# Kernel tuning notes

Hardware: AMD Instinct MI355X
Metric: run time of the kernel (lower is better)

Reference implementation:

```python
import jax, jax.numpy as jnp
import numpy as np

EMBED = 768
CROSS = 512
HEADS = 12
HDIM = EMBED // HEADS
FFN = 4 * EMBED
B, S, L = 8, 1024, 256
EPS = 1e-5


def setup_inputs() -> dict:
    key = jax.random.key(0)
    ks = iter(jax.random.split(key, 40))
    r = lambda shape, s=0.02: jax.random.normal(next(ks), shape, dtype=jnp.float32) * s
    inp = {
        'hidden_state': jax.random.normal(next(ks), (B, S, EMBED), dtype=jnp.float32),
        'context': jax.random.normal(next(ks), (B, L, CROSS), dtype=jnp.float32),
        # cross_norm
        'cn_g': jnp.ones((EMBED,), jnp.float32), 'cn_b': jnp.zeros((EMBED,), jnp.float32),
        # cross attention projections
        'wq_c': r((EMBED, EMBED)), 'bq_c': jnp.zeros((EMBED,), jnp.float32),
        'wk_c': r((CROSS, EMBED)), 'bk_c': jnp.zeros((EMBED,), jnp.float32),
        'wv_c': r((CROSS, EMBED)), 'bv_c': jnp.zeros((EMBED,), jnp.float32),
        'wo_c': r((EMBED, EMBED)), 'bo_c': jnp.zeros((EMBED,), jnp.float32),
        'bias_c': r((HEADS, S, L)),  # relative position bias (cross)
        # self_norm
        'sn_g': jnp.ones((EMBED,), jnp.float32), 'sn_b': jnp.zeros((EMBED,), jnp.float32),
        # self attention projections
        'wq_s': r((EMBED, EMBED)), 'bq_s': jnp.zeros((EMBED,), jnp.float32),
        'wk_s': r((EMBED, EMBED)), 'bk_s': jnp.zeros((EMBED,), jnp.float32),
        'wv_s': r((EMBED, EMBED)), 'bv_s': jnp.zeros((EMBED,), jnp.float32),
        'wo_s': r((EMBED, EMBED)), 'bo_s': jnp.zeros((EMBED,), jnp.float32),
        'bias_s': r((HEADS, S, S)),  # relative position bias (self)
        # ffn_norm
        'fn_g': jnp.ones((EMBED,), jnp.float32), 'fn_b': jnp.zeros((EMBED,), jnp.float32),
        # FFN
        'w1': r((EMBED, FFN)), 'b1': jnp.zeros((FFN,), jnp.float32),
        'w2': r((FFN, EMBED)), 'b2': jnp.zeros((EMBED,), jnp.float32),
    }
    return inp


def _ln(x, g, b):
    mu = jnp.mean(x, axis=-1, keepdims=True)
    var = jnp.mean(jnp.square(x - mu), axis=-1, keepdims=True)
    return (x - mu) * jax.lax.rsqrt(var + EPS) * g + b


def _heads(x):  # [B,T,E] -> [B,H,T,D]
    b, t, _ = x.shape
    return x.reshape(b, t, HEADS, HDIM).transpose(0, 2, 1, 3)


def _attn(xq, xkv, wq, bq, wk, bk, wv, bv, wo, bo, bias):
    q = _heads(xq @ wq + bq)
    k = _heads(xkv @ wk + bk)
    v = _heads(xkv @ wv + bv)
    scale = 1.0 / jnp.sqrt(jnp.asarray(HDIM, q.dtype))
    scores = jnp.einsum('bhqd,bhkd->bhqk', q, k) * scale + bias[None]
    p = jax.nn.softmax(scores, axis=-1)
    o = jnp.einsum('bhqk,bhkd->bhqd', p, v)
    b_, _, t, _ = o.shape
    o = o.transpose(0, 2, 1, 3).reshape(b_, t, EMBED)
    return o @ wo + bo


def reference(hidden_state, context, cn_g, cn_b, wq_c, bq_c, wk_c, bk_c, wv_c, bv_c,
              wo_c, bo_c, bias_c, sn_g, sn_b, wq_s, bq_s, wk_s, bk_s, wv_s, bv_s,
              wo_s, bo_s, bias_s, fn_g, fn_b, w1, b1, w2, b2):
    h = _attn(_ln(hidden_state, cn_g, cn_b), context,
              wq_c, bq_c, wk_c, bk_c, wv_c, bv_c, wo_c, bo_c, bias_c) + hidden_state
    h = _attn(_ln(h, sn_g, sn_b), _ln(h, sn_g, sn_b),
              wq_s, bq_s, wk_s, bk_s, wv_s, bv_s, wo_s, bo_s, bias_s) + h
    y = _ln(h, fn_g, fn_b)
    y = jax.nn.gelu(y @ w1 + b1) @ w2 + b2  # NOTE: original has no residual after FFN
    return y
```

## Files before the change

### kernel.cpp

```cpp
#include <hip/hip_runtime.h>
#include <hip/hip_bf16.h>
#include <math.h>

#define EMBED 768
#define CROSS 512
#define HEADS 12
#define HDIM  64
#define FFN_DIM 3072
#define BATCH 8
#define SEQ   1024
#define CTX   256
#define LN_EPS 1e-5f

using f32x4 = __attribute__((ext_vector_type(4))) float;
using s16x8 = __attribute__((ext_vector_type(8))) short;

__device__ __forceinline__ unsigned short f2bf(float f) {
    union { float f; unsigned u; } x{f};
    const unsigned r = x.u + 0x7fffu + ((x.u >> 16) & 1u);
    return (unsigned short)(r >> 16);
}

__device__ __forceinline__ void gl16(const void* g, void* l) {
    __builtin_amdgcn_global_load_lds(
        (const __attribute__((address_space(1))) void*)g,
        (__attribute__((address_space(3))) void*)l, 16, 0, 0);
}

__device__ __forceinline__ float gelu_f(float x) {
    const float c = 0.7978845608028654f;
    return 0.5f * x * (1.0f + tanhf(c * (x + 0.044715f * x * x * x)));
}

__global__ __launch_bounds__(256) void transpose_cast_kernel(
    const float* __restrict__ W, unsigned short* __restrict__ WT, int K, int N)
{
    __shared__ float T[32][33];
    const int k0 = blockIdx.y * 32, n0 = blockIdx.x * 32;
    const int t = threadIdx.x;
    const int r = t >> 3, c4 = (t & 7) * 4;
    const float4 v = *(const float4*)(W + (size_t)(k0 + r) * N + n0 + c4);
    T[r][c4 + 0] = v.x; T[r][c4 + 1] = v.y; T[r][c4 + 2] = v.z; T[r][c4 + 3] = v.w;
    __syncthreads();
    ushort4 o;
    o.x = f2bf(T[c4 + 0][r]); o.y = f2bf(T[c4 + 1][r]);
    o.z = f2bf(T[c4 + 2][r]); o.w = f2bf(T[c4 + 3][r]);
    *(ushort4*)(WT + (size_t)(n0 + r) * K + k0 + c4) = o;
}

__global__ __launch_bounds__(256) void cast_bf16_kernel(
    const float* __restrict__ x, unsigned short* __restrict__ y, int n)
{
    const int i = (blockIdx.x * 256 + threadIdx.x) * 4;
    if (i < n) {
        const float4 v = *(const float4*)(x + i);
        ushort4 o{f2bf(v.x), f2bf(v.y), f2bf(v.z), f2bf(v.w)};
        *(ushort4*)(y + i) = o;
    }
}

__global__ __launch_bounds__(256) void ln_kernel(
    const float* __restrict__ x, const float* __restrict__ g,
    const float* __restrict__ beta, unsigned short* __restrict__ y)
{
    __shared__ float red[256];
    const size_t row = blockIdx.x;
    const float* xr = x + row * EMBED;
    const int t = threadIdx.x;

    float v0 = xr[t], v1 = xr[t + 256], v2 = xr[t + 512];

    red[t] = v0 + v1 + v2;
    __syncthreads();
    for (int off = 128; off > 0; off >>= 1) {
        if (t < off) red[t] += red[t + off];
        __syncthreads();
    }
    const float mu = red[0] * (1.0f / (float)EMBED);
    __syncthreads();

    const float d0 = v0 - mu, d1 = v1 - mu, d2 = v2 - mu;
    red[t] = d0 * d0 + d1 * d1 + d2 * d2;
    __syncthreads();
    for (int off = 128; off > 0; off >>= 1) {
        if (t < off) red[t] += red[t + off];
        __syncthreads();
    }
    const float var = red[0] * (1.0f / (float)EMBED);
    const float rstd = rsqrtf(var + LN_EPS);

    unsigned short* yr = y + row * EMBED;
    yr[t]       = f2bf(d0 * rstd * g[t]       + beta[t]);
    yr[t + 256] = f2bf(d1 * rstd * g[t + 256] + beta[t + 256]);
    yr[t + 512] = f2bf(d2 * rstd * g[t + 512] + beta[t + 512]);
}

template <int MODE, int DO_GELU>
__global__ __launch_bounds__(256) void gemm_mfma_kernel(
    const unsigned short* __restrict__ A,
    const unsigned short* __restrict__ WT,
    const float* __restrict__ bias,
    const float* __restrict__ resid,
    void* __restrict__ Cv, int M, int N, int K, int sklog)
{
    __shared__ unsigned short As[128][32];
    __shared__ unsigned short Bs[128][32];

    const int t = threadIdx.x;
    const int l = t & 63;
    const int w = t >> 6;
    const int m0 = blockIdx.y * 128;
    const int n0 = blockIdx.x * 128;
    const int wm = (w >> 1) * 64;
    const int wn = (w & 1) * 64;

    const int sr = t >> 2;
    const int sc = t & 3;

    f32x4 acc[4][4] = {};

    const unsigned short* Ap0 = A  + (size_t)(m0 + sr) * K + sc * 8;
    const unsigned short* Ap1 = Ap0 + (size_t)64 * K;
    const unsigned short* Bp0 = WT + (size_t)(n0 + sr) * K + sc * 8;
    const unsigned short* Bp1 = Bp0 + (size_t)64 * K;

    const int fr = l & 15;
    const int kb = (l >> 4) * 8;

    for (int k0 = 0; k0 < K; k0 += 32) {
        gl16(Ap0 + k0, &As[sr][sc * 8]);
        gl16(Ap1 + k0, &As[sr + 64][sc * 8]);
        gl16(Bp0 + k0, &Bs[sr][sc * 8]);
        gl16(Bp1 + k0, &Bs[sr + 64][sc * 8]);
        __syncthreads();

        s16x8 af[4], bf[4];
#pragma unroll
        for (int i = 0; i < 4; ++i) af[i] = *(const s16x8*)&As[wm + i * 16 + fr][kb];
#pragma unroll
        for (int j = 0; j < 4; ++j) bf[j] = *(const s16x8*)&Bs[wn + j * 16 + fr][kb];
#pragma unroll
        for (int i = 0; i < 4; ++i)
#pragma unroll
            for (int j = 0; j < 4; ++j)
                acc[i][j] = __builtin_amdgcn_mfma_f32_16x16x32_bf16(
                    af[i], bf[j], acc[i][j], 0, 0, 0);
        __syncthreads();
    }

    const int rg = (l >> 4) * 4;
#pragma unroll
    for (int j = 0; j < 4; ++j) {
        const int col = n0 + wn + j * 16 + fr;
        const float bia = bias[col];
#pragma unroll
        for (int i = 0; i < 4; ++i) {
#pragma unroll
            for (int r = 0; r < 4; ++r) {
                const int row = m0 + wm + i * 16 + rg + r;
                float v = acc[i][j][r] + bia;
                if (resid) v += resid[(size_t)row * N + col];
                if (DO_GELU) v = gelu_f(v);
                if (MODE == 0) {
                    ((float*)Cv)[(size_t)row * N + col] = v;
                } else if (MODE == 1) {
                    ((unsigned short*)Cv)[(size_t)row * N + col] = f2bf(v);
                } else {
                    const int bb = row >> sklog;
                    const int kk = row - (bb << sklog);
                    const int hh = col >> 6;
                    const int dd = col & 63;
                    ((unsigned short*)Cv)[
                        (((size_t)(bb * HEADS + hh) * 64 + dd) << sklog) + kk] = f2bf(v);
                }
            }
        }
    }
}

template <int SK>
__global__ __launch_bounds__(256) void flash_mfma_kernel(
    const unsigned short* __restrict__ Q, const unsigned short* __restrict__ K,
    const unsigned short* __restrict__ VT, const float* __restrict__ bias,
    unsigned short* __restrict__ O, float scale)
{
    __shared__ unsigned short Qs[64][72];
    __shared__ unsigned short Ks[64][72];
    __shared__ unsigned short Vts[64][72];
    __shared__ unsigned short Ps[64][72];

    const int g = blockIdx.x;
    const int L = (g & 7) * 192 + (g >> 3);
    const int b  = L & 7;
    const int qt = (L >> 3) & 15;
    const int h  = L >> 7;
    const int q0 = qt * 64;

    const int t  = threadIdx.x;
    const int l  = t & 63;
    const int w  = t >> 6;
    const int fr = l & 15;
    const int hi = l >> 4;

    const int str = t >> 3;
    const int stc = (t & 7) * 8;

#pragma unroll
    for (int ps = 0; ps < 2; ++ps) {
        const int r = str + ps * 32;
        *(uint4*)&Qs[r][stc] =
            *(const uint4*)(Q + ((size_t)(b * SEQ) + q0 + r) * EMBED + h * HDIM + stc);
    }

    float m_[4], l_[4];
    f32x4 o_[4];
#pragma unroll
    for (int r = 0; r < 4; ++r) { m_[r] = -1e30f; l_[r] = 0.0f; }
#pragma unroll
    for (int n = 0; n < 4; ++n) o_[n] = f32x4{0.f, 0.f, 0.f, 0.f};

    const float* bbase = bias + ((size_t)h * SEQ + q0 + w * 16) * SK;

    for (int k0 = 0; k0 < SK; k0 += 64) {
#pragma unroll
        for (int ps = 0; ps < 2; ++ps) {
            const int r = str + ps * 32;
            *(uint4*)&Ks[r][stc] =
                *(const uint4*)(K + ((size_t)(b * SK) + k0 + r) * EMBED + h * HDIM + stc);
            *(uint4*)&Vts[r][stc] =
                *(const uint4*)(VT + ((size_t)(b * HEADS + h) * 64 + r) * SK + k0 + stc);
        }
        __syncthreads();

        f32x4 s[4] = {};
#pragma unroll
        for (int ks = 0; ks < 2; ++ks) {
            const s16x8 aq = *(const s16x8*)&Qs[w * 16 + fr][ks * 32 + hi * 8];
#pragma unroll
            for (int j = 0; j < 4; ++j) {
                const s16x8 bk = *(const s16x8*)&Ks[j * 16 + fr][ks * 32 + hi * 8];
                s[j] = __builtin_amdgcn_mfma_f32_16x16x32_bf16(aq, bk, s[j], 0, 0, 0);
            }
        }

        float corr[4];
#pragma unroll
        for (int r = 0; r < 4; ++r) {
            const float* br = bbase + (size_t)(hi * 4 + r) * SK + k0 + fr;
            float v0 = s[0][r] * scale + br[0];
            float v1 = s[1][r] * scale + br[16];
            float v2 = s[2][r] * scale + br[32];
            float v3 = s[3][r] * scale + br[48];
            float mx = fmaxf(fmaxf(v0, v1), fmaxf(v2, v3));
            mx = fmaxf(mx, __shfl_xor(mx, 1));
            mx = fmaxf(mx, __shfl_xor(mx, 2));
            mx = fmaxf(mx, __shfl_xor(mx, 4));
            mx = fmaxf(mx, __shfl_xor(mx, 8));
            const float mnew = fmaxf(m_[r], mx);
            const float c = __expf(m_[r] - mnew);
            m_[r] = mnew;
            const float p0 = __expf(v0 - mnew);
            const float p1 = __expf(v1 - mnew);
            const float p2 = __expf(v2 - mnew);
            const float p3 = __expf(v3 - mnew);
            float psum = p0 + p1 + p2 + p3;
            psum += __shfl_xor(psum, 1);
            psum += __shfl_xor(psum, 2);
            psum += __shfl_xor(psum, 4);
            psum += __shfl_xor(psum, 8);
            l_[r] = l_[r] * c + psum;
            corr[r] = c;
            const int prow = w * 16 + hi * 4 + r;
            Ps[prow][fr]      = f2bf(p0);
            Ps[prow][fr + 16] = f2bf(p1);
            Ps[prow][fr + 32] = f2bf(p2);
            Ps[prow][fr + 48] = f2bf(p3);
        }
#pragma unroll
        for (int n = 0; n < 4; ++n)
#pragma unroll
            for (int r = 0; r < 4; ++r) o_[n][r] *= corr[r];

#pragma unroll
        for (int ks = 0; ks < 2; ++ks) {
            const s16x8 ap = *(const s16x8*)&Ps[w * 16 + fr][ks * 32 + hi * 8];
#pragma unroll
            for (int n = 0; n < 4; ++n) {
                const s16x8 bv = *(const s16x8*)&Vts[n * 16 + fr][ks * 32 + hi * 8];
                o_[n] = __builtin_amdgcn_mfma_f32_16x16x32_bf16(ap, bv, o_[n], 0, 0, 0);
            }
        }
        __syncthreads();
    }

    float inv[4];
#pragma unroll
    for (int r = 0; r < 4; ++r) inv[r] = 1.0f / l_[r];
#pragma unroll
    for (int n = 0; n < 4; ++n)
#pragma unroll
        for (int r = 0; r < 4; ++r)
            O[((size_t)(b * SEQ) + q0 + w * 16 + hi * 4 + r) * EMBED +
              h * HDIM + n * 16 + fr] = f2bf(o_[n][r] * inv[r]);
}

extern "C" void kernel_launch(void* const* d_in, const int* in_sizes, int n_in,
                              void* d_out, int out_size, void* d_ws, size_t ws_size,
                              hipStream_t stream)
{
    const float* hidden  = (const float*)d_in[0];
    const float* context = (const float*)d_in[1];
    const float* cn_g = (const float*)d_in[2];
    const float* cn_b = (const float*)d_in[3];
    const float* wq_c = (const float*)d_in[4];
    const float* bq_c = (const float*)d_in[5];
    const float* wk_c = (const float*)d_in[6];
    const float* bk_c = (const float*)d_in[7];
    const float* wv_c = (const float*)d_in[8];
    const float* bv_c = (const float*)d_in[9];
    const float* wo_c = (const float*)d_in[10];
    const float* bo_c = (const float*)d_in[11];
    const float* bias_c = (const float*)d_in[12];
    const float* sn_g = (const float*)d_in[13];
    const float* sn_b = (const float*)d_in[14];
    const float* wq_s = (const float*)d_in[15];
    const float* bq_s = (const float*)d_in[16];
    const float* wk_s = (const float*)d_in[17];
    const float* bk_s = (const float*)d_in[18];
    const float* wv_s = (const float*)d_in[19];
    const float* bv_s = (const float*)d_in[20];
    const float* wo_s = (const float*)d_in[21];
    const float* bo_s = (const float*)d_in[22];
    const float* bias_s = (const float*)d_in[23];
    const float* fn_g = (const float*)d_in[24];
    const float* fn_b = (const float*)d_in[25];
    const float* w1 = (const float*)d_in[26];
    const float* b1 = (const float*)d_in[27];
    const float* w2 = (const float*)d_in[28];
    const float* b2 = (const float*)d_in[29];

    const size_t NTOK = (size_t)BATCH * SEQ;
    const size_t NCTX = (size_t)BATCH * CTX;
    const size_t TE = NTOK * EMBED;

    char* p = (char*)d_ws;
    float* hbuf = (float*)p;                   p += TE * 4;
    unsigned short* xbuf = (unsigned short*)p; p += TE * 2;
    unsigned short* qbuf = (unsigned short*)p; p += TE * 2;
    unsigned short* kbuf = (unsigned short*)p; p += TE * 2;
    unsigned short* vbuf = (unsigned short*)p; p += TE * 2;
    unsigned short* obuf = (unsigned short*)p; p += TE * 2;
    unsigned short* ctxb = (unsigned short*)p; p += NCTX * CROSS * 2;
    unsigned short* wt_qc = (unsigned short*)p; p += (size_t)EMBED * EMBED * 2;
    unsigned short* wt_kc = (unsigned short*)p; p += (size_t)CROSS * EMBED * 2;
    unsigned short* wt_vc = (unsigned short*)p; p += (size_t)CROSS * EMBED * 2;
    unsigned short* wt_oc = (unsigned short*)p; p += (size_t)EMBED * EMBED * 2;
    unsigned short* wt_qs = (unsigned short*)p; p += (size_t)EMBED * EMBED * 2;
    unsigned short* wt_ks = (unsigned short*)p; p += (size_t)EMBED * EMBED * 2;
    unsigned short* wt_vs = (unsigned short*)p; p += (size_t)EMBED * EMBED * 2;
    unsigned short* wt_os = (unsigned short*)p; p += (size_t)EMBED * EMBED * 2;
    unsigned short* wt_w1 = (unsigned short*)p; p += (size_t)EMBED * FFN_DIM * 2;
    unsigned short* wt_w2 = (unsigned short*)p; p += (size_t)FFN_DIM * EMBED * 2;
    unsigned short* fbuf = qbuf;
    float* out = (float*)d_out;

    const dim3 blk(256);
    const float scale = 0.125f;
    const dim3 agrid(BATCH * (SEQ / 64) * HEADS);

    transpose_cast_kernel<<<dim3(EMBED/32, EMBED/32), blk, 0, stream>>>(wq_c, wt_qc, EMBED, EMBED);
    transpose_cast_kernel<<<dim3(EMBED/32, CROSS/32), blk, 0, stream>>>(wk_c, wt_kc, CROSS, EMBED);
    transpose_cast_kernel<<<dim3(EMBED/32, CROSS/32), blk, 0, stream>>>(wv_c, wt_vc, CROSS, EMBED);
    transpose_cast_kernel<<<dim3(EMBED/32, EMBED/32), blk, 0, stream>>>(wo_c, wt_oc, EMBED, EMBED);
    transpose_cast_kernel<<<dim3(EMBED/32, EMBED/32), blk, 0, stream>>>(wq_s, wt_qs, EMBED, EMBED);
    transpose_cast_kernel<<<dim3(EMBED/32, EMBED/32), blk, 0, stream>>>(wk_s, wt_ks, EMBED, EMBED);
    transpose_cast_kernel<<<dim3(EMBED/32, EMBED/32), blk, 0, stream>>>(wv_s, wt_vs, EMBED, EMBED);
    transpose_cast_kernel<<<dim3(EMBED/32, EMBED/32), blk, 0, stream>>>(wo_s, wt_os, EMBED, EMBED);
    transpose_cast_kernel<<<dim3(FFN_DIM/32, EMBED/32), blk, 0, stream>>>(w1, wt_w1, EMBED, FFN_DIM);
    transpose_cast_kernel<<<dim3(EMBED/32, FFN_DIM/32), blk, 0, stream>>>(w2, wt_w2, FFN_DIM, EMBED);
    cast_bf16_kernel<<<(int)(NCTX * CROSS / 1024), blk, 0, stream>>>(
        context, ctxb, (int)(NCTX * CROSS));

    ln_kernel<<<(int)NTOK, blk, 0, stream>>>(hidden, cn_g, cn_b, xbuf);
    gemm_mfma_kernel<1,0><<<dim3(EMBED/128, NTOK/128), blk, 0, stream>>>(
        xbuf, wt_qc, bq_c, nullptr, qbuf, NTOK, EMBED, EMBED, 0);
    gemm_mfma_kernel<1,0><<<dim3(EMBED/128, NCTX/128), blk, 0, stream>>>(
        ctxb, wt_kc, bk_c, nullptr, kbuf, NCTX, EMBED, CROSS, 0);
    gemm_mfma_kernel<2,0><<<dim3(EMBED/128, NCTX/128), blk, 0, stream>>>(
        ctxb, wt_vc, bv_c, nullptr, vbuf, NCTX, EMBED, CROSS, 8);
    flash_mfma_kernel<CTX><<<agrid, blk, 0, stream>>>(
        qbuf, kbuf, vbuf, bias_c, obuf, scale);
    gemm_mfma_kernel<0,0><<<dim3(EMBED/128, NTOK/128), blk, 0, stream>>>(
        obuf, wt_oc, bo_c, hidden, hbuf, NTOK, EMBED, EMBED, 0);

    ln_kernel<<<(int)NTOK, blk, 0, stream>>>(hbuf, sn_g, sn_b, xbuf);
    gemm_mfma_kernel<1,0><<<dim3(EMBED/128, NTOK/128), blk, 0, stream>>>(
        xbuf, wt_qs, bq_s, nullptr, qbuf, NTOK, EMBED, EMBED, 0);
    gemm_mfma_kernel<1,0><<<dim3(EMBED/128, NTOK/128), blk, 0, stream>>>(
        xbuf, wt_ks, bk_s, nullptr, kbuf, NTOK, EMBED, EMBED, 0);
    gemm_mfma_kernel<2,0><<<dim3(EMBED/128, NTOK/128), blk, 0, stream>>>(
        xbuf, wt_vs, bv_s, nullptr, vbuf, NTOK, EMBED, EMBED, 10);
    flash_mfma_kernel<SEQ><<<agrid, blk, 0, stream>>>(
        qbuf, kbuf, vbuf, bias_s, obuf, scale);
    gemm_mfma_kernel<0,0><<<dim3(EMBED/128, NTOK/128), blk, 0, stream>>>(
        obuf, wt_os, bo_s, hbuf, hbuf, NTOK, EMBED, EMBED, 0);

    ln_kernel<<<(int)NTOK, blk, 0, stream>>>(hbuf, fn_g, fn_b, xbuf);
    gemm_mfma_kernel<1,1><<<dim3(FFN_DIM/128, NTOK/128), blk, 0, stream>>>(
        xbuf, wt_w1, b1, nullptr, fbuf, NTOK, FFN_DIM, EMBED, 0);
    gemm_mfma_kernel<0,0><<<dim3(EMBED/128, NTOK/128), blk, 0, stream>>>(
        fbuf, wt_w2, b2, nullptr, out, NTOK, EMBED, FFN_DIM, 0);
}
```

Before: 828.2 us.

## Fuse QKV projections into one GEMM and prefetch K/V tiles in flash attention

Concatenates the transposed K/V (cross) and Q/K/V (self) weights so that each projection set runs as a single wider GEMM launch, with per-block routing of bias and output (V written transposed). The flash attention kernel now loads the next K/V tile into registers while computing on the current one, and loads the bias values for a tile into registers up front. This removes launch overhead and underfilled grids from the small projection GEMMs and hides global-load latency in attention, at the cost of more registers and an extra barrier per iteration.

```diff
diff --git a/kernel.cpp b/kernel.cpp
--- a/kernel.cpp
+++ b/kernel.cpp
@@ -101,7 +101,7 @@
     const unsigned short* __restrict__ WT,
     const float* __restrict__ bias,
     const float* __restrict__ resid,
-    void* __restrict__ Cv, int M, int N, int K, int sklog)
+    void* __restrict__ Cv, int M, int N, int K)
 {
     __shared__ unsigned short As[128][32];
     __shared__ unsigned short Bs[128][32];
@@ -163,15 +163,91 @@
                 if (DO_GELU) v = gelu_f(v);
                 if (MODE == 0) {
                     ((float*)Cv)[(size_t)row * N + col] = v;
-                } else if (MODE == 1) {
+                } else {
                     ((unsigned short*)Cv)[(size_t)row * N + col] = f2bf(v);
-                } else {
+                }
+            }
+        }
+    }
+}
+
+__global__ __launch_bounds__(256) void gemm_qkv_kernel(
+    const unsigned short* __restrict__ A,
+    const unsigned short* __restrict__ WT,
+    const float* __restrict__ b0, const float* __restrict__ b1,
+    const float* __restrict__ b2,
+    unsigned short* __restrict__ out0, unsigned short* __restrict__ out1,
+    unsigned short* __restrict__ vt,
+    int M, int K, int sklog, int vpart)
+{
+    __shared__ unsigned short As[128][32];
+    __shared__ unsigned short Bs[128][32];
+
+    const int t = threadIdx.x;
+    const int l = t & 63;
+    const int w = t >> 6;
+    const int m0 = blockIdx.y * 128;
+    const int n0 = blockIdx.x * 128;
+    const int part = n0 / 768;
+    const int nl0 = n0 - part * 768;
+    const float* bias = (part == 0) ? b0 : ((part == 1) ? b1 : b2);
+    const int wm = (w >> 1) * 64;
+    const int wn = (w & 1) * 64;
+
+    const int sr = t >> 2;
+    const int sc = t & 3;
+
+    f32x4 acc[4][4] = {};
+
+    const unsigned short* Ap0 = A  + (size_t)(m0 + sr) * K + sc * 8;
+    const unsigned short* Ap1 = Ap0 + (size_t)64 * K;
+    const unsigned short* Bp0 = WT + (size_t)(n0 + sr) * K + sc * 8;
+    const unsigned short* Bp1 = Bp0 + (size_t)64 * K;
+
+    const int fr = l & 15;
+    const int kb = (l >> 4) * 8;
+
+    for (int k0 = 0; k0 < K; k0 += 32) {
+        gl16(Ap0 + k0, &As[sr][sc * 8]);
+        gl16(Ap1 + k0, &As[sr + 64][sc * 8]);
+        gl16(Bp0 + k0, &Bs[sr][sc * 8]);
+        gl16(Bp1 + k0, &Bs[sr + 64][sc * 8]);
+        __syncthreads();
+
+        s16x8 af[4], bf[4];
+#pragma unroll
+        for (int i = 0; i < 4; ++i) af[i] = *(const s16x8*)&As[wm + i * 16 + fr][kb];
+#pragma unroll
+        for (int j = 0; j < 4; ++j) bf[j] = *(const s16x8*)&Bs[wn + j * 16 + fr][kb];
+#pragma unroll
+        for (int i = 0; i < 4; ++i)
+#pragma unroll
+            for (int j = 0; j < 4; ++j)
+                acc[i][j] = __builtin_amdgcn_mfma_f32_16x16x32_bf16(
+                    af[i], bf[j], acc[i][j], 0, 0, 0);
+        __syncthreads();
+    }
+
+    const int rg = (l >> 4) * 4;
+    unsigned short* outp = (part == 0) ? out0 : out1;
+#pragma unroll
+    for (int j = 0; j < 4; ++j) {
+        const int nl = nl0 + wn + j * 16 + fr;
+        const float bia = bias[nl];
+#pragma unroll
+        for (int i = 0; i < 4; ++i) {
+#pragma unroll
+            for (int r = 0; r < 4; ++r) {
+                const int row = m0 + wm + i * 16 + rg + r;
+                const float v = acc[i][j][r] + bia;
+                if (part == vpart) {
                     const int bb = row >> sklog;
                     const int kk = row - (bb << sklog);
-                    const int hh = col >> 6;
-                    const int dd = col & 63;
-                    ((unsigned short*)Cv)[
-                        (((size_t)(bb * HEADS + hh) * 64 + dd) << sklog) + kk] = f2bf(v);
+                    const int hh = nl >> 6;
+                    const int dd = nl & 63;
+                    vt[(((size_t)(bb * HEADS + hh) * 64 + dd) << sklog) + kk] = f2bf(v);
+                } else {
+                    outp[(size_t)row * 768 + nl] = f2bf(v);
                 }
             }
         }
@@ -205,6 +281,8 @@
     const int str = t >> 3;
     const int stc = (t & 7) * 8;
 
+    const unsigned short* Kbase = K + (size_t)(b * SK) * EMBED + h * HDIM + stc;
+
 #pragma unroll
     for (int ps = 0; ps < 2; ++ps) {
         const int r = str + ps * 32;
@@ -212,6 +290,20 @@
             *(const uint4*)(Q + ((size_t)(b * SEQ) + q0 + r) * EMBED + h * HDIM + stc);
     }
 
+    uint4 kreg[2], vreg[2];
+#pragma unroll
+    for (int ps = 0; ps < 2; ++ps) {
+        const int r = str + ps * 32;
+        kreg[ps] = *(const uint4*)(Kbase + (size_t)r * EMBED);
+        vreg[ps] = *(const uint4*)(VT + ((size_t)(b * HEADS + h) * 64 + r) * SK + stc);
+    }
+#pragma unroll
+    for (int ps = 0; ps < 2; ++ps) {
+        const int r = str + ps * 32;
+        *(uint4*)&Ks[r][stc]  = kreg[ps];
+        *(uint4*)&Vts[r][stc] = vreg[ps];
+    }
+
     float m_[4], l_[4];
     f32x4 o_[4];
 #pragma unroll
@@ -220,17 +312,25 @@
     for (int n = 0; n < 4; ++n) o_[n] = f32x4{0.f, 0.f, 0.f, 0.f};
 
     const float* bbase = bias + ((size_t)h * SEQ + q0 + w * 16) * SK;
+    __syncthreads();
 
     for (int k0 = 0; k0 < SK; k0 += 64) {
-#pragma unroll
-        for (int ps = 0; ps < 2; ++ps) {
-            const int r = str + ps * 32;
-            *(uint4*)&Ks[r][stc] =
-                *(const uint4*)(K + ((size_t)(b * SK) + k0 + r) * EMBED + h * HDIM + stc);
-            *(uint4*)&Vts[r][stc] =
-                *(const uint4*)(VT + ((size_t)(b * HEADS + h) * 64 + r) * SK + k0 + stc);
-        }
-        __syncthreads();
+        const int kn = k0 + 64;
+        if (kn < SK) {
+#pragma unroll
+            for (int ps = 0; ps < 2; ++ps) {
+                const int r = str + ps * 32;
+                kreg[ps] = *(const uint4*)(Kbase + (size_t)(kn + r) * EMBED);
+                vreg[ps] = *(const uint4*)(VT + ((size_t)(b * HEADS + h) * 64 + r) * SK + kn + stc);
+            }
+        }
+
+        float bre[4][4];
+#pragma unroll
+        for (int r = 0; r < 4; ++r)
+#pragma unroll
+            for (int j = 0; j < 4; ++j)
+                bre[r][j] = bbase[(size_t)(hi * 4 + r) * SK + k0 + fr + 16 * j];
 
         f32x4 s[4] = {};
 #pragma unroll
@@ -246,11 +346,10 @@
         float corr[4];
 #pragma unroll
         for (int r = 0; r < 4; ++r) {
-            const float* br = bbase + (size_t)(hi * 4 + r) * SK + k0 + fr;
-            float v0 = s[0][r] * scale + br[0];
-            float v1 = s[1][r] * scale + br[16];
-            float v2 = s[2][r] * scale + br[32];
-            float v3 = s[3][r] * scale + br[48];
+            float v0 = s[0][r] * scale + bre[r][0];
+            float v1 = s[1][r] * scale + bre[r][1];
+            float v2 = s[2][r] * scale + bre[r][2];
+            float v3 = s[3][r] * scale + bre[r][3];
             float mx = fmaxf(fmaxf(v0, v1), fmaxf(v2, v3));
             mx = fmaxf(mx, __shfl_xor(mx, 1));
             mx = fmaxf(mx, __shfl_xor(mx, 2));
@@ -291,6 +390,16 @@
             }
         }
         __syncthreads();
+
+        if (kn < SK) {
+#pragma unroll
+            for (int ps = 0; ps < 2; ++ps) {
+                const int r = str + ps * 32;
+                *(uint4*)&Ks[r][stc]  = kreg[ps];
+                *(uint4*)&Vts[r][stc] = vreg[ps];
+            }
+            __syncthreads();
+        }
     }
 
     float inv[4];
@@ -351,16 +460,13 @@
     unsigned short* vbuf = (unsigned short*)p; p += TE * 2;
     unsigned short* obuf = (unsigned short*)p; p += TE * 2;
     unsigned short* ctxb = (unsigned short*)p; p += NCTX * CROSS * 2;
-    unsigned short* wt_qc = (unsigned short*)p; p += (size_t)EMBED * EMBED * 2;
-    unsigned short* wt_kc = (unsigned short*)p; p += (size_t)CROSS * EMBED * 2;
-    unsigned short* wt_vc = (unsigned short*)p; p += (size_t)CROSS * EMBED * 2;
-    unsigned short* wt_oc = (unsigned short*)p; p += (size_t)EMBED * EMBED * 2;
-    unsigned short* wt_qs = (unsigned short*)p; p += (size_t)EMBED * EMBED * 2;
-    unsigned short* wt_ks = (unsigned short*)p; p += (size_t)EMBED * EMBED * 2;
-    unsigned short* wt_vs = (unsigned short*)p; p += (size_t)EMBED * EMBED * 2;
-    unsigned short* wt_os = (unsigned short*)p; p += (size_t)EMBED * EMBED * 2;
-    unsigned short* wt_w1 = (unsigned short*)p; p += (size_t)EMBED * FFN_DIM * 2;
-    unsigned short* wt_w2 = (unsigned short*)p; p += (size_t)FFN_DIM * EMBED * 2;
+    unsigned short* wt_qc   = (unsigned short*)p; p += (size_t)EMBED * EMBED * 2;
+    unsigned short* wt_kvc  = (unsigned short*)p; p += (size_t)2 * EMBED * CROSS * 2;
+    unsigned short* wt_oc   = (unsigned short*)p; p += (size_t)EMBED * EMBED * 2;
+    unsigned short* wt_qkvs = (unsigned short*)p; p += (size_t)3 * EMBED * EMBED * 2;
+    unsigned short* wt_os   = (unsigned short*)p; p += (size_t)EMBED * EMBED * 2;
+    unsigned short* wt_w1   = (unsigned short*)p; p += (size_t)EMBED * FFN_DIM * 2;
+    unsigned short* wt_w2   = (unsigned short*)p; p += (size_t)FFN_DIM * EMBED * 2;
     unsigned short* fbuf = qbuf;
     float* out = (float*)d_out;
 
@@ -369,12 +475,15 @@
     const dim3 agrid(BATCH * (SEQ / 64) * HEADS);
 
     transpose_cast_kernel<<<dim3(EMBED/32, EMBED/32), blk, 0, stream>>>(wq_c, wt_qc, EMBED, EMBED);
-    transpose_cast_kernel<<<dim3(EMBED/32, CROSS/32), blk, 0, stream>>>(wk_c, wt_kc, CROSS, EMBED);
-    transpose_cast_kernel<<<dim3(EMBED/32, CROSS/32), blk, 0, stream>>>(wv_c, wt_vc, CROSS, EMBED);
+    transpose_cast_kernel<<<dim3(EMBED/32, CROSS/32), blk, 0, stream>>>(wk_c, wt_kvc, CROSS, EMBED);
+    transpose_cast_kernel<<<dim3(EMBED/32, CROSS/32), blk, 0, stream>>>(
+        wv_c, wt_kvc + (size_t)EMBED * CROSS, CROSS, EMBED);
     transpose_cast_kernel<<<dim3(EMBED/32, EMBED/32), blk, 0, stream>>>(wo_c, wt_oc, EMBED, EMBED);
-    transpose_cast_kernel<<<dim3(EMBED/32, EMBED/32), blk, 0, stream>>>(wq_s, wt_qs, EMBED, EMBED);
-    transpose_cast_kernel<<<dim3(EMBED/32, EMBED/32), blk, 0, stream>>>(wk_s, wt_ks, EMBED, EMBED);
-    transpose_cast_kernel<<<dim3(EMBED/32, EMBED/32), blk, 0, stream>>>(wv_s, wt_vs, EMBED, EMBED);
+    transpose_cast_kernel<<<dim3(EMBED/32, EMBED/32), blk, 0, stream>>>(wq_s, wt_qkvs, EMBED, EMBED);
+    transpose_cast_kernel<<<dim3(EMBED/32, EMBED/32), blk, 0, stream>>>(
+        wk_s, wt_qkvs + (size_t)EMBED * EMBED, EMBED, EMBED);
+    transpose_cast_kernel<<<dim3(EMBED/32, EMBED/32), blk, 0, stream>>>(
+        wv_s, wt_qkvs + (size_t)2 * EMBED * EMBED, EMBED, EMBED);
     transpose_cast_kernel<<<dim3(EMBED/32, EMBED/32), blk, 0, stream>>>(wo_s, wt_os, EMBED, EMBED);
     transpose_cast_kernel<<<dim3(FFN_DIM/32, EMBED/32), blk, 0, stream>>>(w1, wt_w1, EMBED, FFN_DIM);
     transpose_cast_kernel<<<dim3(EMBED/32, FFN_DIM/32), blk, 0, stream>>>(w2, wt_w2, FFN_DIM, EMBED);
@@ -383,31 +492,27 @@
 
     ln_kernel<<<(int)NTOK, blk, 0, stream>>>(hidden, cn_g, cn_b, xbuf);
     gemm_mfma_kernel<1,0><<<dim3(EMBED/128, NTOK/128), blk, 0, stream>>>(
-        xbuf, wt_qc, bq_c, nullptr, qbuf, NTOK, EMBED, EMBED, 0);
-    gemm_mfma_kernel<1,0><<<dim3(EMBED/128, NCTX/128), blk, 0, stream>>>(
-        ctxb, wt_kc, bk_c, nullptr, kbuf, NCTX, EMBED, CROSS, 0);
-    gemm_mfma_kernel<2,0><<<dim3(EMBED/128, NCTX/128), blk, 0, stream>>>(
-        ctxb, wt_vc, bv_c, nullptr, vbuf, NCTX, EMBED, CROSS, 8);
+        xbuf, wt_qc, bq_c, nullptr, qbuf, NTOK, EMBED, EMBED);
+    gemm_qkv_kernel<<<dim3(2*EMBED/128, NCTX/128), blk, 0, stream>>>(
+        ctxb, wt_kvc, bk_c, bv_c, nullptr, kbuf, nullptr, vbuf,
+        NCTX, CROSS, 8, 1);
     flash_mfma_kernel<CTX><<<agrid, blk, 0, stream>>>(
         qbuf, kbuf, vbuf, bias_c, obuf, scale);
     gemm_mfma_kernel<0,0><<<dim3(EMBED/128, NTOK/128), blk, 0, stream>>>(
-        obuf, wt_oc, bo_c, hidden, hbuf, NTOK, EMBED, EMBED, 0);
+        obuf, wt_oc, bo_c, hidden, hbuf, NTOK, EMBED, EMBED);
 
     ln_kernel<<<(int)NTOK, blk, 0, stream>>>(hbuf, sn_g, sn_b, xbuf);
-    gemm_mfma_kernel<1,0><<<dim3(EMBED/128, NTOK/128), blk, 0, stream>>>(
-        xbuf, wt_qs, bq_s, nullptr, qbuf, NTOK, EMBED, EMBED, 0);
-    gemm_mfma_kernel<1,0><<<dim3(EMBED/128, NTOK/128), blk, 0, stream>>>(
-        xbuf, wt_ks, bk_s, nullptr, kbuf, NTOK, EMBED, EMBED, 0);
-    gemm_mfma_kernel<2,0><<<dim3(EMBED/128, NTOK/128), blk, 0, stream>>>(
-        xbuf, wt_vs, bv_s, nullptr, vbuf, NTOK, EMBED, EMBED, 10);
+    gemm_qkv_kernel<<<dim3(3*EMBED/128, NTOK/128), blk, 0, stream>>>(
+        xbuf, wt_qkvs, bq_s, bk_s, bv_s, qbuf, kbuf, vbuf,
+        NTOK, EMBED, 10, 2);
     flash_mfma_kernel<SEQ><<<agrid, blk, 0, stream>>>(
         qbuf, kbuf, vbuf, bias_s, obuf, scale);
     gemm_mfma_kernel<0,0><<<dim3(EMBED/128, NTOK/128), blk, 0, stream>>>(
-        obuf, wt_os, bo_s, hbuf, hbuf, NTOK, EMBED, EMBED, 0);
+        obuf, wt_os, bo_s, hbuf, hbuf, NTOK, EMBED, EMBED);
 
     ln_kernel<<<(int)NTOK, blk, 0, stream>>>(hbuf, fn_g, fn_b, xbuf);
     gemm_mfma_kernel<1,1><<<dim3(FFN_DIM/128, NTOK/128), blk, 0, stream>>>(
-        xbuf, wt_w1, b1, nullptr, fbuf, NTOK, FFN_DIM, EMBED, 0);
+        xbuf, wt_w1, b1, nullptr, fbuf, NTOK, FFN_DIM, EMBED);
     gemm_mfma_kernel<0,0><<<dim3(EMBED/128, NTOK/128), blk, 0, stream>>>(
-        fbuf, wt_w2, b2, nullptr, out, NTOK, EMBED, FFN_DIM, 0);
-}
+        fbuf, wt_w2, b2, nullptr, out, NTOK, EMBED, FFN_DIM);
+}
```

Result: no change. 812.0 us (-1.9%).
